# Kernel tuning notes

Hardware: AMD Instinct MI355X
Metric: run time of the kernel (lower is better)

Reference implementation:

```python
import jax, jax.numpy as jnp
import numpy as np

N_NODES = 100000
N_EDGES = 3200000
FEAT = 256
HIDDEN = 32
EMBED = 16


def gcn_conv(x, row, col, ew, W, b, num_nodes):
    """PyG GCNConv (add_self_loops=True, normalize=True) in eval mode.
    x: [N, Fin], row/col: [E] (source, target), ew: [E], W: [Fout, Fin], b: [Fout].
    """
    # add self loops with weight 1 (fill_value=1.0)
    loop = jnp.arange(num_nodes, dtype=row.dtype)
    row_f = jnp.concatenate([row, loop])
    col_f = jnp.concatenate([col, loop])
    ew_f = jnp.concatenate([ew, jnp.ones((num_nodes,), dtype=ew.dtype)])
    # symmetric normalization: deg over target (col) for source_to_target flow
    deg = jax.ops.segment_sum(ew_f, col_f, num_segments=num_nodes)
    dis = jnp.where(deg > 0, jax.lax.rsqrt(deg), 0.0)  # deg^{-1/2}, inf -> 0
    norm = dis[row_f] * ew_f * dis[col_f]  # [E+N]
    h = x @ W.T  # [N, Fout] -- linear (no bias) before propagate
    msg = h[row_f] * norm[:, None]  # gather + weight messages
    out = jax.ops.segment_sum(msg, col_f, num_segments=num_nodes)  # scatter-add
    return out + b


def setup_inputs() -> dict:
    key = jax.random.key(0)
    ks = jax.random.split(key, 8)
    x = jax.random.normal(ks[0], (N_NODES, FEAT), dtype=jnp.float32)
    ei = jax.random.randint(ks[1], (2, N_EDGES), 0, N_NODES, dtype=jnp.int64)
    ew = jax.random.uniform(ks[2], (N_EDGES,), dtype=jnp.float32)
    s1 = 1.0 / np.sqrt(FEAT)
    s2 = 1.0 / np.sqrt(HIDDEN)
    W1 = jax.random.uniform(ks[3], (HIDDEN, FEAT), minval=-s1, maxval=s1, dtype=jnp.float32)
    b1 = jax.random.uniform(ks[4], (HIDDEN,), minval=-s1, maxval=s1, dtype=jnp.float32)
    W2 = jax.random.uniform(ks[5], (EMBED, HIDDEN), minval=-s2, maxval=s2, dtype=jnp.float32)
    b2 = jax.random.uniform(ks[6], (EMBED,), minval=-s2, maxval=s2, dtype=jnp.float32)
    return {"x": x, "ei": ei, "ew": ew, "W1": W1, "b1": b1, "W2": W2, "b2": b2}


def reference(x, ei, ew, W1, b1, W2, b2):
    row, col = ei[0], ei[1]
    h = gcn_conv(x, row, col, ew, W1, b1, N_NODES)
    h = jax.nn.relu(h)
    # Dropout(0.25) and DropEdge(0.8) are identity in eval mode
    return gcn_conv(h, row, col, ew, W2, b2, N_NODES)
```

## Files before the change

### kernel.cpp

```cpp
#include <hip/hip_runtime.h>
#include <hip/hip_bf16.h>

#define N_NODES 100000
#define N_EDGES 3200000
#define FEAT 256
#define HIDDEN 32
#define EMBED 16
#define NPB 128
#define NBIN ((N_NODES + NPB - 1) / NPB)
#define CAPB 4608
#define OCAP 8192
#define GR 128
#define G1N 32
#define G1CAP 2048
#define G2N 64
#define G2CAP 3072
#define PEPB 3072
#define PBLK ((N_EDGES + PEPB - 1) / PEPB)
#define OMS 784
#define RPT 5
#define NSK (NPB * 8)

__global__ __launch_bounds__(256, 4) void k_part(
        const int* __restrict__ row, const int* __restrict__ col,
        const float* __restrict__ ew, int* __restrict__ offm,
        int2* __restrict__ chunks, int* __restrict__ ocur) {
    __shared__ int2 sed[PEPB];
    __shared__ int shist[NBIN];
    __shared__ int scur[NBIN];
    const int tid = threadIdx.x;
    const int blk = blockIdx.x;
    const int e0 = blk * PEPB;
    const int ne = min(PEPB, N_EDGES - e0);
    if (blk == 0 && tid == 0) *ocur = 0;

    for (int i = tid; i < NBIN; i += 256) shist[i] = 0;
    __syncthreads();
    for (int i = tid; i < ne; i += 256) atomicAdd(&shist[col[e0 + i] >> 7], 1);
    __syncthreads();
    int l[4];
    int s = 0;
#pragma unroll
    for (int k = 0; k < 4; ++k) {
        int b = tid * 4 + k;
        l[k] = (b < NBIN) ? shist[b] : 0;
        s += l[k];
    }
    scur[tid] = s;
    __syncthreads();
    for (int d = 1; d < 256; d <<= 1) {
        int t = (tid >= d) ? scur[tid - d] : 0;
        __syncthreads();
        scur[tid] += t;
        __syncthreads();
    }
    int ex = scur[tid] - s;
    __syncthreads();
#pragma unroll
    for (int k = 0; k < 4; ++k) {
        int b = tid * 4 + k;
        if (b < NBIN) {
            shist[b] = ex;
            scur[b] = ex;
            ex += l[k];
        }
    }
    __syncthreads();
    for (int b = tid; b < NBIN; b += 256) offm[blk * OMS + b] = shist[b];
    if (tid == 0) offm[blk * OMS + NBIN] = ne;
    for (int i = tid; i < ne; i += 256) {
        int e = e0 + i;
        int c = col[e];
        int b = c >> 7;
        int p = atomicAdd(&scur[b], 1);
        sed[p] = make_int2(((c & (NPB - 1)) << 17) | row[e], __float_as_int(ew[e]));
    }
    __syncthreads();
    for (int i = tid; i < ne; i += 256) chunks[(size_t)blk * PEPB + i] = sed[i];
}

__global__ __launch_bounds__(256) void k_build(
        const int* __restrict__ offm, const int2* __restrict__ chunks,
        int2* __restrict__ binned, float* __restrict__ deg,
        int2* __restrict__ off2, int* __restrict__ binTot,
        int* __restrict__ ocur, int4* __restrict__ olist) {
    __shared__ int2 se[CAPB];
    __shared__ int scnt[NSK], scur2[NSK];
    __shared__ float sdeg[NPB];
    __shared__ int spart[256];
    const int bin = blockIdx.x, tid = threadIdx.x;
    const size_t base = (size_t)bin * CAPB;

    for (int i = tid; i < NSK; i += 256) scnt[i] = 0;
    for (int i = tid; i < NPB; i += 256) sdeg[i] = 0.f;
    int st[RPT], ln[RPT];
    int s = 0;
#pragma unroll
    for (int r = 0; r < RPT; ++r) {
        int k = tid * RPT + r;
        int a = 0, b2 = 0;
        if (k < PBLK) {
            a = offm[k * OMS + bin];
            b2 = offm[k * OMS + bin + 1];
        }
        st[r] = a;
        ln[r] = b2 - a;
        s += ln[r];
    }
    spart[tid] = s;
    __syncthreads();
    for (int d = 1; d < 256; d <<= 1) {
        int t = (tid >= d) ? spart[tid - d] : 0;
        __syncthreads();
        spart[tid] += t;
        __syncthreads();
    }
    int ex = spart[tid] - s;
    const int nTot = spart[255];
    const int n = min(nTot, CAPB);
    int dp = ex;
#pragma unroll
    for (int r = 0; r < RPT; ++r) {
        int k = tid * RPT + r;
        if (k < PBLK) {
            const int2* src = chunks + (size_t)k * PEPB + st[r];
            for (int j = 0; j < ln[r]; ++j) {
                int2 v = src[j];
                int lc = v.x >> 17;
                int dst = dp + j;
                if (dst < CAPB) {
                    se[dst] = v;
                    atomicAdd(&scnt[lc * 8 + ((v.x & 0x1FFFF) >> 14)], 1);
                    atomicAdd(&sdeg[lc], __int_as_float(v.y));
                } else {
                    int q = atomicAdd(ocur, 1);
                    if (q < OCAP)
                        olist[q] = make_int4(v.x & 0x1FFFF, bin * NPB + lc, v.y, 0);
                }
            }
            dp += ln[r];
        }
    }
    __syncthreads();
    int l0 = scnt[tid * 4], l1 = scnt[tid * 4 + 1],
        l2 = scnt[tid * 4 + 2], l3 = scnt[tid * 4 + 3];
    int s2 = l0 + l1 + l2 + l3;
    spart[tid] = s2;
    __syncthreads();
    for (int d = 1; d < 256; d <<= 1) {
        int t = (tid >= d) ? spart[tid - d] : 0;
        __syncthreads();
        spart[tid] += t;
        __syncthreads();
    }
    int ex2 = spart[tid] - s2;
    scnt[tid * 4] = ex2;
    scnt[tid * 4 + 1] = ex2 + l0;
    scnt[tid * 4 + 2] = ex2 + l0 + l1;
    scnt[tid * 4 + 3] = ex2 + l0 + l1 + l2;
    __syncthreads();
    for (int i = tid; i < NSK; i += 256) scur2[i] = scnt[i];
    __syncthreads();
    if (tid < NPB) {
        int node = bin * NPB + tid;
        if (node < N_NODES) {
            int stn = scnt[tid * 8];
            int en = (tid == NPB - 1) ? n : scnt[(tid + 1) * 8];
            off2[node] = make_int2((int)base + stn, en - stn);
            deg[node] = sdeg[tid] + 1.0f;
        }
    }
    if (tid == 0) binTot[bin] = n;
    __syncthreads();
    for (int i = tid; i < n; i += 256) {
        int2 v = se[i];
        int lc = v.x >> 17, src2 = v.x & 0x1FFFF;
        int p = atomicAdd(&scur2[lc * 8 + (src2 >> 14)], 1);
        binned[base + p] = make_int2(src2, v.y);
    }
}

__global__ void k_degover(const int* __restrict__ ocur, const int4* __restrict__ olist,
                          float* __restrict__ deg) {
    int p = blockIdx.x * blockDim.x + threadIdx.x;
    int n = min(*ocur, OCAP);
    if (p < n) { int4 t = olist[p]; unsafeAtomicAdd(&deg[t.y], __int_as_float(t.z)); }
}

__global__ void k_dis(float* __restrict__ deg) {
    int i = blockIdx.x * blockDim.x + threadIdx.x;
    if (i < N_NODES) {
        float d = deg[i];
        deg[i] = (d > 0.0f) ? rsqrtf(d) : 0.0f;
    }
}

__global__ void k_wnorm(const int* __restrict__ binTot, int2* __restrict__ csr,
                        const float* __restrict__ dis) {
    int bin = blockIdx.x;
    int n = binTot[bin];
    size_t base = (size_t)bin * CAPB;
    for (int i = threadIdx.x; i < n; i += 256) {
        int2 v = csr[base + i];
        float w = __int_as_float(v.y) * dis[v.x];
        csr[base + i] = make_int2(v.x, __float_as_int(w));
    }
}

__global__ __launch_bounds__(256) void k_gemm1(
        const float* __restrict__ x, const float* __restrict__ W1,
        float* __restrict__ h) {
    __shared__ float sx[GR][36];
    __shared__ float sw[HIDDEN][260];

    const int tid = threadIdx.x;
    const size_t base = (size_t)blockIdx.x * GR;
    const float4* x4 = (const float4*)x;
    const float4* w4 = (const float4*)W1;
    const int rs = tid >> 3;
    const int ks = tid & 7;

    for (int i = tid; i < HIDDEN * 64; i += 256) {
        int f = i >> 6, kq = i & 63;
        *(float4*)&sw[f][kq * 4] = w4[f * 64 + kq];
    }
    float4 stg[4];
#pragma unroll
    for (int m = 0; m < 4; ++m) {
        int rr = rs + 32 * m;
        stg[m] = make_float4(0.f, 0.f, 0.f, 0.f);
        if (base + rr < N_NODES) stg[m] = x4[(base + rr) * 64 + ks];
    }
#pragma unroll
    for (int m = 0; m < 4; ++m) *(float4*)&sx[rs + 32 * m][ks * 4] = stg[m];
    __syncthreads();

    const int r0 = tid >> 3;
    const int c0 = tid & 7;
    float acc[4][4] = {};

    for (int p = 0; p < 8; ++p) {
        if (p < 7) {
#pragma unroll
            for (int m = 0; m < 4; ++m) {
                int rr = rs + 32 * m;
                stg[m] = make_float4(0.f, 0.f, 0.f, 0.f);
                if (base + rr < N_NODES) stg[m] = x4[(base + rr) * 64 + (p + 1) * 8 + ks];
            }
        }
#pragma unroll
        for (int kq = 0; kq < 8; ++kq) {
            float4 xa[4], wv[4];
#pragma unroll
            for (int m = 0; m < 4; ++m) xa[m] = *(const float4*)&sx[r0 + 32 * m][kq * 4];
#pragma unroll
            for (int j = 0; j < 4; ++j) wv[j] = *(const float4*)&sw[c0 + 8 * j][(p * 8 + kq) * 4];
#pragma unroll
            for (int m = 0; m < 4; ++m)
#pragma unroll
                for (int j = 0; j < 4; ++j)
                    acc[m][j] += xa[m].x * wv[j].x + xa[m].y * wv[j].y +
                                 xa[m].z * wv[j].z + xa[m].w * wv[j].w;
        }
        __syncthreads();
        if (p < 7) {
#pragma unroll
            for (int m = 0; m < 4; ++m) *(float4*)&sx[rs + 32 * m][ks * 4] = stg[m];
            __syncthreads();
        }
    }

#pragma unroll
    for (int m = 0; m < 4; ++m) {
        size_t r = base + r0 + 32 * m;
        if (r < N_NODES) {
#pragma unroll
            for (int j = 0; j < 4; ++j) h[r * HIDDEN + c0 + 8 * j] = acc[m][j];
        }
    }
}

__global__ __launch_bounds__(256) void k_gather1(
        const int2* __restrict__ off2, const int2* __restrict__ csr,
        const float* __restrict__ h, const float* __restrict__ dis,
        const float* __restrict__ b1, const float* __restrict__ W2,
        const int* __restrict__ ocur, const int4* __restrict__ olist,
        float* __restrict__ h2) {
    __shared__ int2 sc[G1CAP];
    __shared__ float sw2[EMBED][HIDDEN + 1];
    __shared__ float sout[G1N][HIDDEN + 1];
    __shared__ int s_start, s_n, s_ov;
    const int tid = threadIdx.x;
    const int node0 = blockIdx.x * G1N;
    if (tid == 0) {
        int2 a = off2[node0];
        int2 b = off2[node0 + G1N - 1];
        s_start = a.x;
        s_n = b.x + b.y - a.x;
        s_ov = *ocur;
    }
    for (int i = tid; i < EMBED * HIDDEN; i += 256) sw2[i >> 5][i & 31] = W2[i];
    __syncthreads();
    const int start = s_start, n = s_n, ov = min(s_ov, OCAP);
    const bool fit = (n <= G1CAP);
    if (fit) for (int i = tid; i < n; i += 256) sc[i] = csr[start + i];
    __syncthreads();

    const int node = node0 + (tid >> 3);
    const int og = tid & 7;
    float d = dis[node];
    float d2 = d * d;
    float4 self = *(const float4*)(h + (size_t)node * HIDDEN + og * 4);
    float4 bv = *(const float4*)(b1 + og * 4);
    float4 acc = make_float4(0.f, 0.f, 0.f, 0.f);

    int2 o = off2[node];
    for (int j = 0; j < o.y; ++j) {
        int2 v = fit ? sc[o.x - start + j] : csr[o.x + j];
        float w = __int_as_float(v.y);
        const float4 hv = *(const float4*)(h + (size_t)v.x * HIDDEN + og * 4);
        acc.x += hv.x * w; acc.y += hv.y * w; acc.z += hv.z * w; acc.w += hv.w * w;
    }
    float4 res = make_float4(acc.x * d + self.x * d2 + bv.x,
                             acc.y * d + self.y * d2 + bv.y,
                             acc.z * d + self.z * d2 + bv.z,
                             acc.w * d + self.w * d2 + bv.w);
    if (ov > 0) {
        for (int q = 0; q < ov; ++q) {
            int4 t = olist[q];
            if (t.y == node) {
                float w = dis[t.x] * __int_as_float(t.z) * d;
                const float4 hv = *(const float4*)(h + (size_t)t.x * HIDDEN + og * 4);
                res.x += hv.x * w; res.y += hv.y * w;
                res.z += hv.z * w; res.w += hv.w * w;
            }
        }
    }
    *(float4*)&sout[tid >> 3][og * 4] =
        make_float4(fmaxf(res.x, 0.f), fmaxf(res.y, 0.f),
                    fmaxf(res.z, 0.f), fmaxf(res.w, 0.f));
    __syncthreads();
    const int n2 = tid >> 3;
    const int f2 = (tid & 7) * 2;
    float a0 = 0.f, a1 = 0.f;
#pragma unroll
    for (int k = 0; k < HIDDEN; ++k) {
        float r = sout[n2][k];
        a0 += r * sw2[f2][k];
        a1 += r * sw2[f2 + 1][k];
    }
    h2[(size_t)(node0 + n2) * EMBED + f2] = a0;
    h2[(size_t)(node0 + n2) * EMBED + f2 + 1] = a1;
}

__global__ __launch_bounds__(256) void k_gather2(
        const int2* __restrict__ off2, const int2* __restrict__ csr,
        const float* __restrict__ h2, const float* __restrict__ dis,
        const float* __restrict__ b2, const int* __restrict__ ocur,
        const int4* __restrict__ olist, float* __restrict__ out) {
    __shared__ int2 sc[G2CAP];
    __shared__ int s_start, s_n, s_ov;
    const int tid = threadIdx.x;
    const int node0 = blockIdx.x * G2N;
    const int lastn = min(node0 + G2N, N_NODES) - 1;
    if (tid == 0) {
        int2 a = off2[node0];
        int2 b = off2[lastn];
        s_start = a.x;
        s_n = b.x + b.y - a.x;
        s_ov = *ocur;
    }
    __syncthreads();
    const int start = s_start, n = s_n, ov = min(s_ov, OCAP);
    const bool fit = (n <= G2CAP);
    if (fit) for (int i = tid; i < n; i += 256) sc[i] = csr[start + i];
    __syncthreads();

    const int node = node0 + (tid >> 2);
    const int og = tid & 3;
    if (node >= N_NODES) return;
    float d = dis[node];
    float d2 = d * d;
    float4 self = *(const float4*)(h2 + (size_t)node * EMBED + og * 4);
    float4 bv = *(const float4*)(b2 + og * 4);
    float4 acc = make_float4(0.f, 0.f, 0.f, 0.f);

    int2 o = off2[node];
    for (int j = 0; j < o.y; ++j) {
        int2 v = fit ? sc[o.x - start + j] : csr[o.x + j];
        float w = __int_as_float(v.y);
        const float4 hv = *(const float4*)(h2 + (size_t)v.x * EMBED + og * 4);
        acc.x += hv.x * w; acc.y += hv.y * w; acc.z += hv.z * w; acc.w += hv.w * w;
    }
    float4 res = make_float4(acc.x * d + self.x * d2 + bv.x,
                             acc.y * d + self.y * d2 + bv.y,
                             acc.z * d + self.z * d2 + bv.z,
                             acc.w * d + self.w * d2 + bv.w);
    if (ov > 0) {
        for (int q = 0; q < ov; ++q) {
            int4 t = olist[q];
            if (t.y == node) {
                float w = dis[t.x] * __int_as_float(t.z) * d;
                const float4 hv = *(const float4*)(h2 + (size_t)t.x * EMBED + og * 4);
                res.x += hv.x * w; res.y += hv.y * w;
                res.z += hv.z * w; res.w += hv.w * w;
            }
        }
    }
    *(float4*)(out + (size_t)node * EMBED + og * 4) = res;
}

extern "C" void kernel_launch(void* const* d_in, const int* in_sizes, int n_in,
                              void* d_out, int out_size, void* d_ws, size_t ws_size,
                              hipStream_t stream) {
    const float* x  = (const float*)d_in[0];
    const int*   ei = (const int*)d_in[1];
    const float* ew = (const float*)d_in[2];
    const float* W1 = (const float*)d_in[3];
    const float* b1 = (const float*)d_in[4];
    const float* W2 = (const float*)d_in[5];
    const float* b2 = (const float*)d_in[6];
    float* out = (float*)d_out;

    const int* row = ei;
    const int* col = ei + N_EDGES;

    int2*  off2   = (int2*)d_ws;
    int2*  binned = off2 + N_NODES;
    float* deg    = (float*)(binned + (size_t)NBIN * CAPB);
    int*   binTot = (int*)(deg + N_NODES);
    int*   offm   = binTot + 784;
    int*   ocur   = offm + (size_t)PBLK * OMS;
    int4*  olist  = (int4*)(ocur + 4);
    void*  big    = (void*)(olist + OCAP);
    int2*  chunks = (int2*)big;
    float* h      = (float*)big;
    float* h2     = h + (size_t)N_NODES * HIDDEN;

    const int B = 256;
    const int gN = (N_NODES + B - 1) / B;
    const int gO = (OCAP + B - 1) / B;

    k_part<<<PBLK, B, 0, stream>>>(row, col, ew, offm, chunks, ocur);
    k_build<<<NBIN, B, 0, stream>>>(offm, chunks, binned, deg, off2, binTot, ocur, olist);
    k_degover<<<gO, B, 0, stream>>>(ocur, olist, deg);
    k_dis<<<gN, B, 0, stream>>>(deg);
    k_wnorm<<<NBIN, B, 0, stream>>>(binTot, binned, deg);
    k_gemm1<<<(N_NODES + GR - 1) / GR, B, 0, stream>>>(x, W1, h);
    k_gather1<<<N_NODES / G1N, B, 0, stream>>>(off2, binned, h, deg, b1, W2, ocur, olist, h2);
    k_gather2<<<(N_NODES + G2N - 1) / G2N, B, 0, stream>>>(off2, binned, h2, deg, b2, ocur, olist, out);
}
```

Measured before the change: 290.5 us.

## Fold source-side degree normalization into GEMM and gather outputs, drop k_wnorm

Removes the k_wnorm kernel, which rescaled every edge weight by dis[src]. Instead, each node's transformed features are pre-scaled by dis[node] in the GEMM epilogue and in the layer-2 projection inside gather1. The gathers then use the raw edge weights, and the self-loop and overflow terms are simplified to match. This saves one full read-modify-write pass over the edge array and one launch, at the cost of a per-row multiply in the epilogues.

```diff
diff --git a/kernel.cpp b/kernel.cpp
--- a/kernel.cpp
+++ b/kernel.cpp
@@ -82,8 +82,7 @@
 __global__ __launch_bounds__(256) void k_build(
         const int* __restrict__ offm, const int2* __restrict__ chunks,
         int2* __restrict__ binned, float* __restrict__ deg,
-        int2* __restrict__ off2, int* __restrict__ binTot,
-        int* __restrict__ ocur, int4* __restrict__ olist) {
+        int2* __restrict__ off2, int* __restrict__ ocur, int4* __restrict__ olist) {
     __shared__ int2 se[CAPB];
     __shared__ int scnt[NSK], scur2[NSK];
     __shared__ float sdeg[NPB];
@@ -170,7 +169,6 @@
             deg[node] = sdeg[tid] + 1.0f;
         }
     }
-    if (tid == 0) binTot[bin] = n;
     __syncthreads();
     for (int i = tid; i < n; i += 256) {
         int2 v = se[i];
@@ -195,21 +193,9 @@
     }
 }
 
-__global__ void k_wnorm(const int* __restrict__ binTot, int2* __restrict__ csr,
-                        const float* __restrict__ dis) {
-    int bin = blockIdx.x;
-    int n = binTot[bin];
-    size_t base = (size_t)bin * CAPB;
-    for (int i = threadIdx.x; i < n; i += 256) {
-        int2 v = csr[base + i];
-        float w = __int_as_float(v.y) * dis[v.x];
-        csr[base + i] = make_int2(v.x, __float_as_int(w));
-    }
-}
-
 __global__ __launch_bounds__(256) void k_gemm1(
         const float* __restrict__ x, const float* __restrict__ W1,
-        float* __restrict__ h) {
+        const float* __restrict__ dis, float* __restrict__ h) {
     __shared__ float sx[GR][36];
     __shared__ float sw[HIDDEN][260];
 
@@ -274,8 +260,9 @@
     for (int m = 0; m < 4; ++m) {
         size_t r = base + r0 + 32 * m;
         if (r < N_NODES) {
-#pragma unroll
-            for (int j = 0; j < 4; ++j) h[r * HIDDEN + c0 + 8 * j] = acc[m][j];
+            float ds = dis[r];
+#pragma unroll
+            for (int j = 0; j < 4; ++j) h[r * HIDDEN + c0 + 8 * j] = acc[m][j] * ds;
         }
     }
 }
@@ -309,7 +296,6 @@
     const int node = node0 + (tid >> 3);
     const int og = tid & 7;
     float d = dis[node];
-    float d2 = d * d;
     float4 self = *(const float4*)(h + (size_t)node * HIDDEN + og * 4);
     float4 bv = *(const float4*)(b1 + og * 4);
     float4 acc = make_float4(0.f, 0.f, 0.f, 0.f);
@@ -321,15 +307,15 @@
         const float4 hv = *(const float4*)(h + (size_t)v.x * HIDDEN + og * 4);
         acc.x += hv.x * w; acc.y += hv.y * w; acc.z += hv.z * w; acc.w += hv.w * w;
     }
-    float4 res = make_float4(acc.x * d + self.x * d2 + bv.x,
-                             acc.y * d + self.y * d2 + bv.y,
-                             acc.z * d + self.z * d2 + bv.z,
-                             acc.w * d + self.w * d2 + bv.w);
+    float4 res = make_float4((acc.x + self.x) * d + bv.x,
+                             (acc.y + self.y) * d + bv.y,
+                             (acc.z + self.z) * d + bv.z,
+                             (acc.w + self.w) * d + bv.w);
     if (ov > 0) {
         for (int q = 0; q < ov; ++q) {
             int4 t = olist[q];
             if (t.y == node) {
-                float w = dis[t.x] * __int_as_float(t.z) * d;
+                float w = __int_as_float(t.z) * d;
                 const float4 hv = *(const float4*)(h + (size_t)t.x * HIDDEN + og * 4);
                 res.x += hv.x * w; res.y += hv.y * w;
                 res.z += hv.z * w; res.w += hv.w * w;
@@ -349,8 +335,8 @@
         a0 += r * sw2[f2][k];
         a1 += r * sw2[f2 + 1][k];
     }
-    h2[(size_t)(node0 + n2) * EMBED + f2] = a0;
-    h2[(size_t)(node0 + n2) * EMBED + f2 + 1] = a1;
+    h2[(size_t)(node0 + n2) * EMBED + f2] = a0 * d;
+    h2[(size_t)(node0 + n2) * EMBED + f2 + 1] = a1 * d;
 }
 
 __global__ __launch_bounds__(256) void k_gather2(
@@ -380,7 +366,6 @@
     const int og = tid & 3;
     if (node >= N_NODES) return;
     float d = dis[node];
-    float d2 = d * d;
     float4 self = *(const float4*)(h2 + (size_t)node * EMBED + og * 4);
     float4 bv = *(const float4*)(b2 + og * 4);
     float4 acc = make_float4(0.f, 0.f, 0.f, 0.f);
@@ -392,15 +377,15 @@
         const float4 hv = *(const float4*)(h2 + (size_t)v.x * EMBED + og * 4);
         acc.x += hv.x * w; acc.y += hv.y * w; acc.z += hv.z * w; acc.w += hv.w * w;
     }
-    float4 res = make_float4(acc.x * d + self.x * d2 + bv.x,
-                             acc.y * d + self.y * d2 + bv.y,
-                             acc.z * d + self.z * d2 + bv.z,
-                             acc.w * d + self.w * d2 + bv.w);
+    float4 res = make_float4((acc.x + self.x) * d + bv.x,
+                             (acc.y + self.y) * d + bv.y,
+                             (acc.z + self.z) * d + bv.z,
+                             (acc.w + self.w) * d + bv.w);
     if (ov > 0) {
         for (int q = 0; q < ov; ++q) {
             int4 t = olist[q];
             if (t.y == node) {
-                float w = dis[t.x] * __int_as_float(t.z) * d;
+                float w = __int_as_float(t.z) * d;
                 const float4 hv = *(const float4*)(h2 + (size_t)t.x * EMBED + og * 4);
                 res.x += hv.x * w; res.y += hv.y * w;
                 res.z += hv.z * w; res.w += hv.w * w;
@@ -428,8 +413,7 @@
     int2*  off2   = (int2*)d_ws;
     int2*  binned = off2 + N_NODES;
     float* deg    = (float*)(binned + (size_t)NBIN * CAPB);
-    int*   binTot = (int*)(deg + N_NODES);
-    int*   offm   = binTot + 784;
+    int*   offm   = (int*)(deg + N_NODES);
     int*   ocur   = offm + (size_t)PBLK * OMS;
     int4*  olist  = (int4*)(ocur + 4);
     void*  big    = (void*)(olist + OCAP);
@@ -442,11 +426,10 @@
     const int gO = (OCAP + B - 1) / B;
 
     k_part<<<PBLK, B, 0, stream>>>(row, col, ew, offm, chunks, ocur);
-    k_build<<<NBIN, B, 0, stream>>>(offm, chunks, binned, deg, off2, binTot, ocur, olist);
+    k_build<<<NBIN, B, 0, stream>>>(offm, chunks, binned, deg, off2, ocur, olist);
     k_degover<<<gO, B, 0, stream>>>(ocur, olist, deg);
     k_dis<<<gN, B, 0, stream>>>(deg);
-    k_wnorm<<<NBIN, B, 0, stream>>>(binTot, binned, deg);
-    k_gemm1<<<(N_NODES + GR - 1) / GR, B, 0, stream>>>(x, W1, h);
+    k_gemm1<<<(N_NODES + GR - 1) / GR, B, 0, stream>>>(x, W1, deg, h);
     k_gather1<<<N_NODES / G1N, B, 0, stream>>>(off2, binned, h, deg, b1, W2, ocur, olist, h2);
     k_gather2<<<(N_NODES + G2N - 1) / G2N, B, 0, stream>>>(off2, binned, h2, deg, b2, ocur, olist, out);
 }
```

Result: faster. 271.1 us (-6.7%).
